# Kernel tuning notes

Hardware: AMD Instinct MI355X
Metric: run time of the kernel (lower is better)

Reference implementation:

```python
import jax, jax.numpy as jnp
import numpy as np

D_MODEL = 1024
N_HEADS = 16
DEPTH = D_MODEL // N_HEADS
B, S = 2, 2048


def setup_inputs() -> dict:
    key = jax.random.key(0)
    ks = jax.random.split(key, 11)
    scale = 1.0 / np.sqrt(D_MODEL)
    return {
        "q": jax.random.normal(ks[0], (B, S, D_MODEL), jnp.float32),
        "k": jax.random.normal(ks[1], (B, S, D_MODEL), jnp.float32),
        "v": jax.random.normal(ks[2], (B, S, D_MODEL), jnp.float32),
        "wq": jax.random.normal(ks[3], (D_MODEL, D_MODEL), jnp.float32) * scale,
        "bq": jnp.zeros((D_MODEL,), jnp.float32),
        "wk": jax.random.normal(ks[4], (D_MODEL, D_MODEL), jnp.float32) * scale,
        "bk": jnp.zeros((D_MODEL,), jnp.float32),
        "wv": jax.random.normal(ks[5], (D_MODEL, D_MODEL), jnp.float32) * scale,
        "bv": jnp.zeros((D_MODEL,), jnp.float32),
        "wo": jax.random.normal(ks[6], (D_MODEL, D_MODEL), jnp.float32) * scale,
        "bo": jnp.zeros((D_MODEL,), jnp.float32),
    }


def _mha(q, k, v, wq, bq, wk, bk, wv, bv, wo, bo):
    b, s, _ = q.shape
    # separate QKV projections
    qh = (q @ wq + bq).reshape(b, s, N_HEADS, DEPTH).transpose(0, 2, 1, 3)  # [b,h,s,d]
    kh = (k @ wk + bk).reshape(b, s, N_HEADS, DEPTH).transpose(0, 2, 1, 3)
    vh = (v @ wv + bv).reshape(b, s, N_HEADS, DEPTH).transpose(0, 2, 1, 3)
    # keras.layers.Attention default: UNSCALED dot-product scores, causal mask
    scores = jnp.einsum("bhqd,bhkd->bhqk", qh, kh)  # [b,h,s,s]
    causal = jnp.tril(jnp.ones((s, s), bool))
    scores = jnp.where(causal, scores, jnp.float32(-1e9))
    attn = jax.nn.softmax(scores, axis=-1)
    out = jnp.einsum("bhqk,bhkd->bhqd", attn, vh)  # [b,h,s,d]
    out = out.transpose(0, 2, 1, 3).reshape(b, s, D_MODEL)
    return out @ wo + bo


def reference(q, k, v, wq, bq, wk, bk, wv, bv, wo, bo):
    return _mha(q, k, v, wq, bq, wk, bk, wv, bv, wo, bo)
```

## Files before the change

kernel.cpp:

```cpp
#include <hip/hip_runtime.h>
#include <stdint.h>

#define AS1q __attribute__((address_space(1)))
#define AS3q __attribute__((address_space(3)))

typedef unsigned short US;
typedef __bf16 bf16x8 __attribute__((ext_vector_type(8)));
typedef float f32x4 __attribute__((ext_vector_type(4)));
typedef float f32x16 __attribute__((ext_vector_type(16)));
typedef float f32x2 __attribute__((ext_vector_type(2)));
typedef __bf16 bf16x2 __attribute__((ext_vector_type(2)));

#define LOG2E 1.44269504088896340736f

__device__ __forceinline__ US f2bf(float f) {
  union { float f; uint32_t u; } c; c.f = f;
  uint32_t u = c.u;
  return (US)((u + 0x7fffu + ((u >> 16) & 1u)) >> 16);
}

__device__ __forceinline__ bf16x8 asb(uint4 u) {
  union { uint4 u; bf16x8 b; } c; c.u = u; return c.b;
}

__device__ __forceinline__ uint32_t pk2(float a, float b) {
  f32x2 fv; fv[0] = a; fv[1] = b;
  bf16x2 bb = __builtin_convertvector(fv, bf16x2);
  union { bf16x2 b; uint32_t u; } c; c.b = bb; return c.u;
}

__device__ __forceinline__ void gload16(const void* g, void* l) {
  __builtin_amdgcn_global_load_lds((AS1q void*)(void*)g, (AS3q void*)l, 16, 0, 0);
}

__global__ void prep_kernel(const float* __restrict__ q, const float* __restrict__ k,
                            const float* __restrict__ v,
                            const float* __restrict__ w0, const float* __restrict__ w1,
                            const float* __restrict__ w2, const float* __restrict__ w3,
                            US* __restrict__ qb, US* __restrict__ kb, US* __restrict__ vb,
                            US* __restrict__ t0, US* __restrict__ t1,
                            US* __restrict__ t2, US* __restrict__ t3) {
  __shared__ US T[64 * 68];
  const int bx = blockIdx.x;
  const int t = threadIdx.x;
  if (bx < 6144) {
    const int ten = bx >> 11, chunk = bx & 2047;
    const float* s; US* d;
    if (ten == 0)      { s = q; d = qb; }
    else if (ten == 1) { s = k; d = kb; }
    else               { s = v; d = vb; }
    int i = (chunk * 256 + t) * 8;
    float4 f0 = *(const float4*)&s[i];
    float4 f1 = *(const float4*)&s[i + 4];
    ushort4 u0, u1;
    u0.x = f2bf(f0.x); u0.y = f2bf(f0.y); u0.z = f2bf(f0.z); u0.w = f2bf(f0.w);
    u1.x = f2bf(f1.x); u1.y = f2bf(f1.y); u1.z = f2bf(f1.z); u1.w = f2bf(f1.w);
    *(ushort4*)&d[i] = u0;
    *(ushort4*)&d[i + 4] = u1;
    return;
  }
  const int idx = bx - 6144;
  const int wsel = idx >> 8, rem = idx & 255;
  const int n0 = (rem & 15) * 64, k0 = (rem >> 4) * 64;
  const float* W; US* Wt;
  if (wsel == 0)      { W = w0; Wt = t0; }
  else if (wsel == 1) { W = w1; Wt = t1; }
  else if (wsel == 2) { W = w2; Wt = t2; }
  else                { W = w3; Wt = t3; }
#pragma unroll
  for (int it = 0; it < 4; ++it) {
    int p = t + it * 256;
    int row = p >> 4, c4 = (p & 15) * 4;
    float4 f = *(const float4*)&W[(k0 + row) * 1024 + n0 + c4];
    ushort4 u;
    u.x = f2bf(f.x); u.y = f2bf(f.y); u.z = f2bf(f.z); u.w = f2bf(f.w);
    *(ushort4*)&T[row * 68 + c4] = u;
  }
  __syncthreads();
#pragma unroll
  for (int it = 0; it < 4; ++it) {
    int p = t + it * 256;
    int rn = p >> 4, ck = (p & 15) * 4;
    ushort4 o;
    o.x = T[(ck + 0) * 68 + rn];
    o.y = T[(ck + 1) * 68 + rn];
    o.z = T[(ck + 2) * 68 + rn];
    o.w = T[(ck + 3) * 68 + rn];
    *(ushort4*)&Wt[(n0 + rn) * 1024 + k0 + ck] = o;
  }
}

template <bool SWAP>
__device__ __forceinline__ void gemm_core(const US* A, const US* Wt,
                                          int m0, int n0, US* As, US* Bs,
                                          f32x4 acc[4][4]) {
  const int tid = threadIdx.x;
  const int wave = tid >> 6, lane = tid & 63;
  const int quad = lane >> 4, l16 = lane & 15;
  const int wm = wave >> 1, wn = wave & 1;
#pragma unroll
  for (int i = 0; i < 4; ++i)
#pragma unroll
    for (int j = 0; j < 4; ++j) acc[i][j] = (f32x4)0.0f;
  const int p = wave * 64 + lane;
  const int arow0 = p >> 2, koff = (p & 3) * 8;
  for (int k0 = 0; k0 < 1024; k0 += 32) {
    gload16(A + (m0 + arow0) * 1024 + k0 + koff, As + wave * 512);
    gload16(A + (m0 + arow0 + 64) * 1024 + k0 + koff, As + 2048 + wave * 512);
    gload16(Wt + (n0 + arow0) * 1024 + k0 + koff, Bs + wave * 512);
    gload16(Wt + (n0 + arow0 + 64) * 1024 + k0 + koff, Bs + 2048 + wave * 512);
    __syncthreads();
    uint4 af[4], bf_[4];
#pragma unroll
    for (int mt = 0; mt < 4; ++mt)
      af[mt] = *(const uint4*)&As[(wm * 64 + mt * 16 + l16) * 32 + quad * 8];
#pragma unroll
    for (int nt = 0; nt < 4; ++nt)
      bf_[nt] = *(const uint4*)&Bs[(wn * 64 + nt * 16 + l16) * 32 + quad * 8];
#pragma unroll
    for (int i = 0; i < 4; ++i)
#pragma unroll
      for (int j = 0; j < 4; ++j) {
        if (SWAP)
          acc[i][j] = __builtin_amdgcn_mfma_f32_16x16x32_bf16(asb(bf_[i]), asb(af[j]),
                                                              acc[i][j], 0, 0, 0);
        else
          acc[i][j] = __builtin_amdgcn_mfma_f32_16x16x32_bf16(asb(af[i]), asb(bf_[j]),
                                                              acc[i][j], 0, 0, 0);
      }
    __syncthreads();
  }
}

__global__ __launch_bounds__(256, 4) void gemm_qkv_kernel(
    const US* __restrict__ qb, const US* __restrict__ kb, const US* __restrict__ vb,
    const US* __restrict__ wfT,
    const float* __restrict__ bq, const float* __restrict__ bk, const float* __restrict__ bv,
    US* __restrict__ qh, US* __restrict__ kh, US* __restrict__ vt) {
  __shared__ __align__(16) US As[4096], Bs[4096];
  const int m0 = blockIdx.x * 128, n0 = blockIdx.y * 128;
  const int which = n0 >> 10;
  const int nl0 = n0 & 1023;
  const US* A = (which == 0) ? qb : (which == 1) ? kb : vb;
  const float* bias = (which == 0) ? bq : (which == 1) ? bk : bv;
  const int tid = threadIdx.x, wave = tid >> 6, lane = tid & 63;
  const int quad = lane >> 4, l16 = lane & 15;
  const int wm = wave >> 1, wn = wave & 1;
  f32x4 acc[4][4];
  if (which == 2) {
    gemm_core<true>(A, wfT, m0, n0, As, Bs, acc);
#pragma unroll
    for (int nt = 0; nt < 4; ++nt) {
      int dg = nl0 + wn * 64 + nt * 16 + quad * 4;
#pragma unroll
      for (int r = 0; r < 4; ++r) {
        int d = dg + r;
        float bval = bias[d];
        int hh = d >> 6, dd = d & 63;
#pragma unroll
        for (int mt = 0; mt < 4; ++mt) {
          int sg = m0 + wm * 64 + mt * 16;
          int bb = sg >> 11, ss = sg & 2047;
          vt[(((size_t)bb * 16 + hh) * 64 + dd) * 2048 + ss + l16] =
              f2bf(acc[nt][mt][r] + bval);
        }
      }
    }
  } else {
    gemm_core<false>(A, wfT, m0, n0, As, Bs, acc);
    US* O = (which == 0) ? qh : kh;
    const float scale = (which == 0) ? LOG2E : 1.0f;
#pragma unroll
    for (int nt = 0; nt < 4; ++nt) {
      int nl = nl0 + wn * 64 + nt * 16 + l16;
      float bval = bias[nl];
      int hh = nl >> 6, d = nl & 63;
#pragma unroll
      for (int mt = 0; mt < 4; ++mt) {
#pragma unroll
        for (int r = 0; r < 4; ++r) {
          int m = m0 + wm * 64 + mt * 16 + quad * 4 + r;
          int bb = m >> 11, s = m & 2047;
          O[((bb * 16 + hh) * 2048 + s) * 64 + d] = f2bf((acc[mt][nt][r] + bval) * scale);
        }
      }
    }
  }
}

__global__ __launch_bounds__(256, 4) void gemm_out_kernel(
    const US* __restrict__ ao, const US* __restrict__ woT,
    const float* __restrict__ bo, float* __restrict__ out) {
  __shared__ __align__(16) US As[4096], Bs[2048];
  const int m0 = blockIdx.x * 128, n0 = blockIdx.y * 64;
  const int tid = threadIdx.x;
  const int wave = tid >> 6, lane = tid & 63;
  const int quad = lane >> 4, l16 = lane & 15;
  f32x4 acc[2][4];
#pragma unroll
  for (int i = 0; i < 2; ++i)
#pragma unroll
    for (int j = 0; j < 4; ++j) acc[i][j] = (f32x4)0.0f;
  const int arow0 = tid >> 2, koff = (tid & 3) * 8;
  for (int k0 = 0; k0 < 1024; k0 += 32) {
    gload16(ao + (m0 + arow0) * 1024 + k0 + koff, As + wave * 512);
    gload16(ao + (m0 + arow0 + 64) * 1024 + k0 + koff, As + 2048 + wave * 512);
    gload16(woT + (n0 + arow0) * 1024 + k0 + koff, Bs + wave * 512);
    __syncthreads();
    uint4 af[2], bf_[4];
#pragma unroll
    for (int mt = 0; mt < 2; ++mt)
      af[mt] = *(const uint4*)&As[(wave * 32 + mt * 16 + l16) * 32 + quad * 8];
#pragma unroll
    for (int nt = 0; nt < 4; ++nt)
      bf_[nt] = *(const uint4*)&Bs[(nt * 16 + l16) * 32 + quad * 8];
#pragma unroll
    for (int mt = 0; mt < 2; ++mt)
#pragma unroll
      for (int nt = 0; nt < 4; ++nt)
        acc[mt][nt] = __builtin_amdgcn_mfma_f32_16x16x32_bf16(asb(af[mt]), asb(bf_[nt]),
                                                              acc[mt][nt], 0, 0, 0);
    __syncthreads();
  }
#pragma unroll
  for (int nt = 0; nt < 4; ++nt) {
    int n = n0 + nt * 16 + l16;
    float bval = bo[n];
#pragma unroll
    for (int mt = 0; mt < 2; ++mt) {
#pragma unroll
      for (int r = 0; r < 4; ++r) {
        int m = m0 + wave * 32 + mt * 16 + quad * 4 + r;
        out[m * 1024 + n] = acc[mt][nt][r] + bval;
      }
    }
  }
}

__global__ __launch_bounds__(512, 4) void attn_kernel(
    const US* __restrict__ qh, const US* __restrict__ kh,
    const US* __restrict__ vt, US* __restrict__ aout) {
  __shared__ __align__(16) char arena[73728];
  US* KsA = (US*)arena;
  US* VsA = (US*)(arena + 32768);
  US* Qs  = (US*)(arena + 65536);
  float* Oex = (float*)arena;
  float* lEx = (float*)(arena + 69632);

  const int tid = threadIdx.x;
  const int wave = tid >> 6, lane = tid & 63;
  const int l31 = lane & 31, lh = lane >> 5;
  const int w_m = wave & 1, w_k = wave >> 1;
  const int bh = blockIdx.x;
  const int b = bh >> 4, h = bh & 15;
  const int jg = blockIdx.y;

  const US* gkb = kh + (size_t)bh * 2048 * 64;
  const US* gvb = vt + (size_t)bh * 64 * 2048;

  for (int ei = 0; ei < 2; ++ei) {
    const int qt = ei ? jg : (31 - jg);
    const int q0 = qt * 64;
    const int nit = (qt >> 1) + 1;
    __syncthreads();
    {
      const US* gq = qh + ((size_t)bh * 2048 + q0) * 64;
      {
        int p = tid;
        int row = p >> 3, c = (p & 7) ^ (row & 7);
        gload16(gq + row * 64 + c * 8, Qs + wave * 512);
      }
#pragma unroll
      for (int ro = 0; ro < 2; ++ro) {
        int p = tid + ro * 512;
        int row = p >> 3, c = (p & 7) ^ (row & 7);
        gload16(gkb + row * 64 + c * 8, KsA + ro * 4096 + wave * 512);
      }
#pragma unroll
      for (int ro = 0; ro < 2; ++ro) {
        int p = tid + ro * 512;
        int row = p >> 4, c = (p & 15) ^ (row & 15);
        gload16(gvb + row * 2048 + c * 8, VsA + ro * 4096 + wave * 512);
      }
    }
    __syncthreads();

    const int qrow = w_m * 32 + l31;
    uint4 bq[4];
#pragma unroll
    for (int s = 0; s < 4; ++s)
      bq[s] = *(const uint4*)&Qs[qrow * 64 + (((2 * s + lh) ^ (qrow & 7)) * 8)];
    const int q_g = q0 + qrow;

    float l_lane = 0.0f;
    f32x16 Oa0 = (f32x16)0.0f, Oa1 = (f32x16)0.0f;

    for (int it = 0; it < nit; ++it) {
      const int cb = it & 1;
      const int kb = it * 128;
      if (it) __syncthreads();
      if (it + 1 < nit) {
        const US* gk = gkb + (kb + 128) * 64;
        const US* gv = gvb + (kb + 128);
        US* kd = KsA + (cb ^ 1) * 8192;
        US* vd = VsA + (cb ^ 1) * 8192;
#pragma unroll
        for (int ro = 0; ro < 2; ++ro) {
          int p = tid + ro * 512;
          int row = p >> 3, c = (p & 7) ^ (row & 7);
          gload16(gk + row * 64 + c * 8, kd + ro * 4096 + wave * 512);
        }
#pragma unroll
        for (int ro = 0; ro < 2; ++ro) {
          int p = tid + ro * 512;
          int row = p >> 4, c = (p & 15) ^ (row & 15);
          gload16(gv + row * 2048 + c * 8, vd + ro * 4096 + wave * 512);
        }
      }
      const US* Kc = KsA + cb * 8192;
      const US* Vc = VsA + cb * 8192;

      f32x16 sa0 = (f32x16)0.0f;
      const int kr0 = w_k * 32 + l31;
#pragma unroll
      for (int s = 0; s < 4; ++s) {
        uint4 ka0 = *(const uint4*)&Kc[kr0 * 64 + (((2 * s + lh) ^ (kr0 & 7)) * 8)];
        sa0 = __builtin_amdgcn_mfma_f32_32x32x16_bf16(asb(ka0), asb(bq[s]), sa0, 0, 0, 0);
      }

      const bool diag = (it == nit - 1);
      float e[16];
      const int kbase = kb + w_k * 32 + 4 * lh;
#pragma unroll
      for (int r = 0; r < 16; ++r) {
        float ev = __builtin_amdgcn_exp2f(sa0[r]);
        if (diag) {
          int key_g = kbase + (r & 3) + 8 * (r >> 2);
          if (key_g > q_g) ev = 0.0f;
        }
        e[r] = ev;
        l_lane += ev;
      }

#pragma unroll
      for (int s2 = 0; s2 < 2; ++s2) {
        uint32_t PA0 = pk2(e[8 * s2 + 0], e[8 * s2 + 1]);
        uint32_t PA1 = pk2(e[8 * s2 + 2], e[8 * s2 + 3]);
        uint32_t PB0 = pk2(e[8 * s2 + 4], e[8 * s2 + 5]);
        uint32_t PB1 = pk2(e[8 * s2 + 6], e[8 * s2 + 7]);
        uint32_t XA0 = (uint32_t)__shfl_xor((int)PA0, 32, 64);
        uint32_t XA1 = (uint32_t)__shfl_xor((int)PA1, 32, 64);
        uint32_t XB0 = (uint32_t)__shfl_xor((int)PB0, 32, 64);
        uint32_t XB1 = (uint32_t)__shfl_xor((int)PB1, 32, 64);
        uint4 bp;
        bp.x = lh ? XB0 : PA0;
        bp.y = lh ? XB1 : PA1;
        bp.z = lh ? PB0 : XA0;
        bp.w = lh ? PB1 : XA1;
        const int c_log = w_k * 4 + s2 * 2 + lh;
        int vr0 = l31;
        uint4 va0 = *(const uint4*)&Vc[vr0 * 128 + ((c_log ^ (vr0 & 15)) * 8)];
        Oa0 = __builtin_amdgcn_mfma_f32_32x32x16_bf16(asb(va0), asb(bp), Oa0, 0, 0, 0);
        int vr1 = 32 + l31;
        uint4 va1 = *(const uint4*)&Vc[vr1 * 128 + ((c_log ^ (vr1 & 15)) * 8)];
        Oa1 = __builtin_amdgcn_mfma_f32_32x32x16_bf16(asb(va1), asb(bp), Oa1, 0, 0, 0);
      }
    }

    float l_q = l_lane + __shfl_xor(l_lane, 32, 64);

    __syncthreads();
    {
      float* myO = Oex + w_k * (64 * 68);
      int q_idx = w_m * 32 + l31;
#pragma unroll
      for (int r = 0; r < 16; ++r) {
        int dr = 4 * lh + (r & 3) + 8 * (r >> 2);
        myO[q_idx * 68 + dr] = Oa0[r];
        myO[q_idx * 68 + 32 + dr] = Oa1[r];
      }
      if (lh == 0) lEx[w_k * 64 + q_idx] = l_q;
    }
    __syncthreads();
    {
      int q_idx = tid >> 3;
      int dseg = (tid & 7) * 8;
      float inv = 1.0f / (lEx[q_idx] + lEx[64 + q_idx] + lEx[128 + q_idx] + lEx[192 + q_idx]);
      union { US s[8]; uint4 v; } ob;
#pragma unroll
      for (int t2 = 0; t2 < 8; ++t2) {
        float o = Oex[q_idx * 68 + dseg + t2]
                + Oex[64 * 68 + q_idx * 68 + dseg + t2]
                + Oex[2 * 64 * 68 + q_idx * 68 + dseg + t2]
                + Oex[3 * 64 * 68 + q_idx * 68 + dseg + t2];
        ob.s[t2] = f2bf(o * inv);
      }
      US* dst = aout + ((size_t)b * 2048 + q0 + q_idx) * 1024 + h * 64 + dseg;
      *(uint4*)dst = ob.v;
    }
  }
}

extern "C" void kernel_launch(void* const* d_in, const int* in_sizes, int n_in,
                              void* d_out, int out_size, void* d_ws, size_t ws_size,
                              hipStream_t stream) {
  const float* q  = (const float*)d_in[0];
  const float* k  = (const float*)d_in[1];
  const float* v  = (const float*)d_in[2];
  const float* wq = (const float*)d_in[3];
  const float* bq = (const float*)d_in[4];
  const float* wk = (const float*)d_in[5];
  const float* bk = (const float*)d_in[6];
  const float* wv = (const float*)d_in[7];
  const float* bv = (const float*)d_in[8];
  const float* wo = (const float*)d_in[9];
  const float* bo = (const float*)d_in[10];
  float* out = (float*)d_out;

  char* ws = (char*)d_ws;
  const size_t MB = 1024 * 1024;
  US* qb  = (US*)(ws + 0 * MB);
  US* kb  = (US*)(ws + 8 * MB);
  US* vb  = (US*)(ws + 16 * MB);
  US* wqT = (US*)(ws + 24 * MB);
  US* wkT = (US*)(ws + 26 * MB);
  US* wvT = (US*)(ws + 28 * MB);
  US* woT = (US*)(ws + 30 * MB);
  US* qh  = (US*)(ws + 32 * MB);
  US* kh  = (US*)(ws + 40 * MB);
  US* vt  = (US*)(ws + 48 * MB);
  US* ao  = (US*)(ws + 56 * MB);

  prep_kernel<<<7168, 256, 0, stream>>>(q, k, v, wq, wk, wv, wo,
                                        qb, kb, vb, wqT, wkT, wvT, woT);
  gemm_qkv_kernel<<<dim3(32, 24), 256, 0, stream>>>(qb, kb, vb, wqT,
                                                    bq, bk, bv, qh, kh, vt);
  attn_kernel<<<dim3(32, 16), 512, 0, stream>>>(qh, kh, vt, ao);
  gemm_out_kernel<<<dim3(32, 16), 256, 0, stream>>>(ao, woT, bo, out);
}
```

Baseline: 205.7 us.

## Double-buffer GEMM LDS staging with swizzle; use permlane32_swap and setprio in attention

Both projection GEMMs now use two LDS buffers and prefetch the next K-slice while computing the current one, so each iteration needs one barrier instead of two. LDS rows are XOR-swizzled to reduce bank conflicts on fragment reads. In attention, four cross-half shuffles plus selects become two permlane32_swap ops, MFMA sections are wrapped in s_setprio, and the occupancy hint drops from 4 to 2 blocks per CU. The cost is doubled LDS in the GEMMs and possibly lower attention occupancy.

```diff
diff --git a/kernel.cpp b/kernel.cpp
--- a/kernel.cpp
+++ b/kernel.cpp
@@ -10,6 +10,7 @@
 typedef float f32x16 __attribute__((ext_vector_type(16)));
 typedef float f32x2 __attribute__((ext_vector_type(2)));
 typedef __bf16 bf16x2 __attribute__((ext_vector_type(2)));
+typedef int v2i __attribute__((ext_vector_type(2)));
 
 #define LOG2E 1.44269504088896340736f
 
@@ -31,6 +32,11 @@
 
 __device__ __forceinline__ void gload16(const void* g, void* l) {
   __builtin_amdgcn_global_load_lds((AS1q void*)(void*)g, (AS3q void*)l, 16, 0, 0);
+}
+
+__device__ __forceinline__ void plswap(uint32_t& a, uint32_t& b) {
+  v2i r = __builtin_amdgcn_permlane32_swap((int)a, (int)b, false, false);
+  a = (uint32_t)r[0]; b = (uint32_t)r[1];
 }
 
 __global__ void prep_kernel(const float* __restrict__ q, const float* __restrict__ k,
@@ -91,9 +97,9 @@
 }
 
 template <bool SWAP>
-__device__ __forceinline__ void gemm_core(const US* A, const US* Wt,
-                                          int m0, int n0, US* As, US* Bs,
-                                          f32x4 acc[4][4]) {
+__device__ __forceinline__ void gemm_core_db(const US* A, const US* Wt,
+                                             int m0, int n0, US* As, US* Bs,
+                                             f32x4 acc[4][4]) {
   const int tid = threadIdx.x;
   const int wave = tid >> 6, lane = tid & 63;
   const int quad = lane >> 4, l16 = lane & 15;
@@ -102,21 +108,41 @@
   for (int i = 0; i < 4; ++i)
 #pragma unroll
     for (int j = 0; j < 4; ++j) acc[i][j] = (f32x4)0.0f;
-  const int p = wave * 64 + lane;
-  const int arow0 = p >> 2, koff = (p & 3) * 8;
-  for (int k0 = 0; k0 < 1024; k0 += 32) {
-    gload16(A + (m0 + arow0) * 1024 + k0 + koff, As + wave * 512);
-    gload16(A + (m0 + arow0 + 64) * 1024 + k0 + koff, As + 2048 + wave * 512);
-    gload16(Wt + (n0 + arow0) * 1024 + k0 + koff, Bs + wave * 512);
-    gload16(Wt + (n0 + arow0 + 64) * 1024 + k0 + koff, Bs + 2048 + wave * 512);
-    __syncthreads();
+
+  const int r0 = tid >> 2;
+  const int pc = tid & 3;
+  const int lc = pc ^ (r0 & 3) ^ ((r0 >> 2) & 3);
+  const US* gA = A + (size_t)(m0 + r0) * 1024 + lc * 8;
+  const US* gB = Wt + (size_t)(n0 + r0) * 1024 + lc * 8;
+  US* lA = As + wave * 512;
+  US* lB = Bs + wave * 512;
+
+#define STGQ(slot, kk)                                          \
+  {                                                             \
+    gload16(gA + (kk), lA + (slot) * 4096);                     \
+    gload16(gA + 64 * 1024 + (kk), lA + (slot) * 4096 + 2048);  \
+    gload16(gB + (kk), lB + (slot) * 4096);                     \
+    gload16(gB + 64 * 1024 + (kk), lB + (slot) * 4096 + 2048);  \
+  }
+
+  STGQ(0, 0);
+  __syncthreads();
+  for (int t = 0; t < 32; ++t) {
+    const int cur = t & 1;
+    if (t + 1 < 32) STGQ(cur ^ 1, (t + 1) * 32);
+    const US* Ab = As + cur * 4096;
+    const US* Bb = Bs + cur * 4096;
     uint4 af[4], bf_[4];
 #pragma unroll
-    for (int mt = 0; mt < 4; ++mt)
-      af[mt] = *(const uint4*)&As[(wm * 64 + mt * 16 + l16) * 32 + quad * 8];
-#pragma unroll
-    for (int nt = 0; nt < 4; ++nt)
-      bf_[nt] = *(const uint4*)&Bs[(wn * 64 + nt * 16 + l16) * 32 + quad * 8];
+    for (int mt = 0; mt < 4; ++mt) {
+      const int row = wm * 64 + mt * 16 + l16;
+      af[mt] = *(const uint4*)&Ab[row * 32 + ((quad ^ (row & 3) ^ ((row >> 2) & 3)) << 3)];
+    }
+#pragma unroll
+    for (int nt = 0; nt < 4; ++nt) {
+      const int row = wn * 64 + nt * 16 + l16;
+      bf_[nt] = *(const uint4*)&Bb[row * 32 + ((quad ^ (row & 3) ^ ((row >> 2) & 3)) << 3)];
+    }
 #pragma unroll
     for (int i = 0; i < 4; ++i)
 #pragma unroll
@@ -130,6 +156,7 @@
       }
     __syncthreads();
   }
+#undef STGQ
 }
 
 __global__ __launch_bounds__(256, 4) void gemm_qkv_kernel(
@@ -137,7 +164,7 @@
     const US* __restrict__ wfT,
     const float* __restrict__ bq, const float* __restrict__ bk, const float* __restrict__ bv,
     US* __restrict__ qh, US* __restrict__ kh, US* __restrict__ vt) {
-  __shared__ __align__(16) US As[4096], Bs[4096];
+  __shared__ __align__(16) US As[2 * 4096], Bs[2 * 4096];
   const int m0 = blockIdx.x * 128, n0 = blockIdx.y * 128;
   const int which = n0 >> 10;
   const int nl0 = n0 & 1023;
@@ -148,7 +175,7 @@
   const int wm = wave >> 1, wn = wave & 1;
   f32x4 acc[4][4];
   if (which == 2) {
-    gemm_core<true>(A, wfT, m0, n0, As, Bs, acc);
+    gemm_core_db<true>(A, wfT, m0, n0, As, Bs, acc);
 #pragma unroll
     for (int nt = 0; nt < 4; ++nt) {
       int dg = nl0 + wn * 64 + nt * 16 + quad * 4;
@@ -167,7 +194,7 @@
       }
     }
   } else {
-    gemm_core<false>(A, wfT, m0, n0, As, Bs, acc);
+    gemm_core_db<false>(A, wfT, m0, n0, As, Bs, acc);
     US* O = (which == 0) ? qh : kh;
     const float scale = (which == 0) ? LOG2E : 1.0f;
 #pragma unroll
@@ -191,7 +218,7 @@
 __global__ __launch_bounds__(256, 4) void gemm_out_kernel(
     const US* __restrict__ ao, const US* __restrict__ woT,
     const float* __restrict__ bo, float* __restrict__ out) {
-  __shared__ __align__(16) US As[4096], Bs[2048];
+  __shared__ __align__(16) US As[2 * 4096], Bs[2 * 2048];
   const int m0 = blockIdx.x * 128, n0 = blockIdx.y * 64;
   const int tid = threadIdx.x;
   const int wave = tid >> 6, lane = tid & 63;
@@ -201,19 +228,40 @@
   for (int i = 0; i < 2; ++i)
 #pragma unroll
     for (int j = 0; j < 4; ++j) acc[i][j] = (f32x4)0.0f;
-  const int arow0 = tid >> 2, koff = (tid & 3) * 8;
-  for (int k0 = 0; k0 < 1024; k0 += 32) {
-    gload16(ao + (m0 + arow0) * 1024 + k0 + koff, As + wave * 512);
-    gload16(ao + (m0 + arow0 + 64) * 1024 + k0 + koff, As + 2048 + wave * 512);
-    gload16(woT + (n0 + arow0) * 1024 + k0 + koff, Bs + wave * 512);
-    __syncthreads();
+
+  const int r0 = tid >> 2;
+  const int pc = tid & 3;
+  const int lc = pc ^ (r0 & 3) ^ ((r0 >> 2) & 3);
+  const US* gA = ao + (size_t)(m0 + r0) * 1024 + lc * 8;
+  const US* gB = woT + (size_t)(n0 + r0) * 1024 + lc * 8;
+  US* lA = As + wave * 512;
+  US* lB = Bs + wave * 512;
+
+#define STGO(slot, kk)                                          \
+  {                                                             \
+    gload16(gA + (kk), lA + (slot) * 4096);                     \
+    gload16(gA + 64 * 1024 + (kk), lA + (slot) * 4096 + 2048);  \
+    gload16(gB + (kk), lB + (slot) * 2048);                     \
+  }
+
+  STGO(0, 0);
+  __syncthreads();
+  for (int t = 0; t < 32; ++t) {
+    const int cur = t & 1;
+    if (t + 1 < 32) STGO(cur ^ 1, (t + 1) * 32);
+    const US* Ab = As + cur * 4096;
+    const US* Bb = Bs + cur * 2048;
     uint4 af[2], bf_[4];
 #pragma unroll
-    for (int mt = 0; mt < 2; ++mt)
-      af[mt] = *(const uint4*)&As[(wave * 32 + mt * 16 + l16) * 32 + quad * 8];
-#pragma unroll
-    for (int nt = 0; nt < 4; ++nt)
-      bf_[nt] = *(const uint4*)&Bs[(nt * 16 + l16) * 32 + quad * 8];
+    for (int mt = 0; mt < 2; ++mt) {
+      const int row = wave * 32 + mt * 16 + l16;
+      af[mt] = *(const uint4*)&Ab[row * 32 + ((quad ^ (row & 3) ^ ((row >> 2) & 3)) << 3)];
+    }
+#pragma unroll
+    for (int nt = 0; nt < 4; ++nt) {
+      const int row = nt * 16 + l16;
+      bf_[nt] = *(const uint4*)&Bb[row * 32 + ((quad ^ (row & 3) ^ ((row >> 2) & 3)) << 3)];
+    }
 #pragma unroll
     for (int mt = 0; mt < 2; ++mt)
 #pragma unroll
@@ -222,6 +270,7 @@
                                                               acc[mt][nt], 0, 0, 0);
     __syncthreads();
   }
+#undef STGO
 #pragma unroll
   for (int nt = 0; nt < 4; ++nt) {
     int n = n0 + nt * 16 + l16;
@@ -237,7 +286,7 @@
   }
 }
 
-__global__ __launch_bounds__(512, 4) void attn_kernel(
+__global__ __launch_bounds__(512, 2) void attn_kernel(
     const US* __restrict__ qh, const US* __restrict__ kh,
     const US* __restrict__ vt, US* __restrict__ aout) {
   __shared__ __align__(16) char arena[73728];
@@ -322,11 +371,13 @@
 
       f32x16 sa0 = (f32x16)0.0f;
       const int kr0 = w_k * 32 + l31;
+      __builtin_amdgcn_s_setprio(1);
 #pragma unroll
       for (int s = 0; s < 4; ++s) {
         uint4 ka0 = *(const uint4*)&Kc[kr0 * 64 + (((2 * s + lh) ^ (kr0 & 7)) * 8)];
         sa0 = __builtin_amdgcn_mfma_f32_32x32x16_bf16(asb(ka0), asb(bq[s]), sa0, 0, 0, 0);
       }
+      __builtin_amdgcn_s_setprio(0);
 
       const bool diag = (it == nit - 1);
       float e[16];
@@ -344,26 +395,22 @@
 
 #pragma unroll
       for (int s2 = 0; s2 < 2; ++s2) {
-        uint32_t PA0 = pk2(e[8 * s2 + 0], e[8 * s2 + 1]);
-        uint32_t PA1 = pk2(e[8 * s2 + 2], e[8 * s2 + 3]);
-        uint32_t PB0 = pk2(e[8 * s2 + 4], e[8 * s2 + 5]);
-        uint32_t PB1 = pk2(e[8 * s2 + 6], e[8 * s2 + 7]);
-        uint32_t XA0 = (uint32_t)__shfl_xor((int)PA0, 32, 64);
-        uint32_t XA1 = (uint32_t)__shfl_xor((int)PA1, 32, 64);
-        uint32_t XB0 = (uint32_t)__shfl_xor((int)PB0, 32, 64);
-        uint32_t XB1 = (uint32_t)__shfl_xor((int)PB1, 32, 64);
-        uint4 bp;
-        bp.x = lh ? XB0 : PA0;
-        bp.y = lh ? XB1 : PA1;
-        bp.z = lh ? PB0 : XA0;
-        bp.w = lh ? PB1 : XA1;
+        uint32_t x0 = pk2(e[8 * s2 + 0], e[8 * s2 + 1]);
+        uint32_t y0 = pk2(e[8 * s2 + 2], e[8 * s2 + 3]);
+        uint32_t z0 = pk2(e[8 * s2 + 4], e[8 * s2 + 5]);
+        uint32_t w0 = pk2(e[8 * s2 + 6], e[8 * s2 + 7]);
+        plswap(x0, z0);
+        plswap(y0, w0);
+        uint4 bp; bp.x = x0; bp.y = y0; bp.z = z0; bp.w = w0;
         const int c_log = w_k * 4 + s2 * 2 + lh;
         int vr0 = l31;
         uint4 va0 = *(const uint4*)&Vc[vr0 * 128 + ((c_log ^ (vr0 & 15)) * 8)];
-        Oa0 = __builtin_amdgcn_mfma_f32_32x32x16_bf16(asb(va0), asb(bp), Oa0, 0, 0, 0);
         int vr1 = 32 + l31;
         uint4 va1 = *(const uint4*)&Vc[vr1 * 128 + ((c_log ^ (vr1 & 15)) * 8)];
+        __builtin_amdgcn_s_setprio(1);
+        Oa0 = __builtin_amdgcn_mfma_f32_32x32x16_bf16(asb(va0), asb(bp), Oa0, 0, 0, 0);
         Oa1 = __builtin_amdgcn_mfma_f32_32x32x16_bf16(asb(va1), asb(bp), Oa1, 0, 0, 0);
+        __builtin_amdgcn_s_setprio(0);
       }
     }
 
```

Result: slower. 216.2 us (+5.1%).
